# Kernel optimization log

Measured on AMD Instinct MI355X. Metric: run time of the kernel, lower is better.

## Reference

```python
import jax, jax.numpy as jnp
import numpy as np


def setup_inputs() -> dict:
    key = jax.random.key(0)
    k1, k2, k3 = jax.random.split(key, 3)
    dim, heads, dim_head, rows = 512, 8, 64, 64
    b, t = 4, 256
    _dim = heads * dim_head
    x = jax.random.normal(k1, (b * rows, t, dim), dtype=jnp.float32)
    # torch nn.Linear weight layout: [out_features, in_features]
    W_qkv = jax.random.normal(k2, (3 * _dim, dim), dtype=jnp.float32) * (dim ** -0.5)
    W0 = jax.random.normal(k3, (dim, _dim), dtype=jnp.float32) * (_dim ** -0.5)
    return {"x": x, "W_qkv": W_qkv, "W0": W0, "rows": rows, "heads": heads}


def reference(x, W_qkv, W0, rows, heads):
    br, t, dim = x.shape
    b = br // rows
    three_dim = W_qkv.shape[0]
    dim_head = three_dim // (3 * heads)
    scale = (rows * dim_head) ** -0.5

    qkv = x @ W_qkv.T  # [(b*rows), t, 3*heads*dim_head]
    # einops '(b rows) t (d k h) -> k b rows h t d': last dim ordered (d, k, h)
    qkv = qkv.reshape(b, rows, t, dim_head, 3, heads)
    qkv = jnp.transpose(qkv, (4, 0, 1, 5, 2, 3))  # [3, b, rows, h, t, d]
    q, k, v = qkv[0], qkv[1], qkv[2]

    # tied-row attention: sum QK^T over rows before a single shared softmax
    scores = jnp.einsum('brhid,brhjd->bhij', q, k) * scale  # [b, h, t, t]
    attn = jax.nn.softmax(scores, axis=-1)
    # broadcast shared attention map back across rows
    out = jnp.einsum('bhij,brhjd->brhid', attn, v)  # [b, rows, h, t, d]
    # 'b rows h t d -> (b rows) t (h d)'
    out = jnp.transpose(out, (0, 1, 3, 2, 4)).reshape(br, t, heads * dim_head)
    return out @ W0.T
```

## Files before the change

### kernel.cpp

```cpp
#include <hip/hip_runtime.h>


typedef short  bf16x8 __attribute__((ext_vector_type(8)));
typedef float  f32x4  __attribute__((ext_vector_type(4)));

#define MFMA16(a,b,c) __builtin_amdgcn_mfma_f32_16x16x32_bf16((a),(b),(c),0,0,0)

__device__ __forceinline__ ushort f2bf(float f) {
  union { float f; unsigned u; } v; v.f = f;
  unsigned r = v.u + 0x7fffu + ((v.u >> 16) & 1u);
  return (ushort)(r >> 16);
}

__device__ __forceinline__ void gload_lds16(const void* g, void* lds) {
  __builtin_amdgcn_global_load_lds(
      (const __attribute__((address_space(1))) void*)g,
      (__attribute__((address_space(3))) void*)lds, 16, 0, 0);
}


__global__ void cast_f32_to_bf16(const float* __restrict__ in,
                                 ushort* __restrict__ out, int n4) {
  int idx = blockIdx.x * blockDim.x + threadIdx.x;
  int stride = gridDim.x * blockDim.x;
  for (int v = idx; v < n4; v += stride) {
    float4 f = reinterpret_cast<const float4*>(in)[v];
    ushort4 o; o.x = f2bf(f.x); o.y = f2bf(f.y); o.z = f2bf(f.z); o.w = f2bf(f.w);
    reinterpret_cast<ushort4*>(out)[v] = o;
  }
}

__global__ void permute_wqkv_k(const float* __restrict__ W, ushort* __restrict__ Wp) {
  int np = blockIdx.x;
  int k = np >> 9, h = (np >> 6) & 7, d = np & 63;
  const float4* s = reinterpret_cast<const float4*>(W + (size_t)(d * 24 + k * 8 + h) * 512);
  ushort4* o = reinterpret_cast<ushort4*>(Wp + (size_t)np * 512);
  for (int c = threadIdx.x; c < 128; c += blockDim.x) {
    float4 f = s[c];
    ushort4 u; u.x = f2bf(f.x); u.y = f2bf(f.y); u.z = f2bf(f.z); u.w = f2bf(f.w);
    o[c] = u;
  }
}


__device__ __forceinline__ void gemm_nt_256x128(
    const ushort* __restrict__ A, const ushort* __restrict__ B,
    int lda, int ldb, int P, int m0, int n0, char* lds, f32x4 (&acc)[8][4]) {
  const int tid = threadIdx.x;
  const int w = tid >> 6, l = tid & 63;
  const int il = l & 15, kl = l >> 4;
  const int wm = w >> 1, wn = w & 1;

  auto stageA = [&](char* buf, int kt) {
#pragma unroll
    for (int c = 0; c < 4; ++c) {
      int rbase = (w << 6) + (c << 4);
      int row = rbase + (l >> 2);
      int s = ((l & 3) - ((row >> 1) & 3)) & 3;
      gload_lds16(A + (size_t)(m0 + row) * lda + (kt << 5) + (s << 3),
                  buf + rbase * 64);
    }
  };
  auto stageB = [&](char* buf, int kt) {
#pragma unroll
    for (int c = 0; c < 2; ++c) {
      int rbase = (w << 5) + (c << 4);
      int row = rbase + (l >> 2);
      int s = ((l & 3) - ((row >> 1) & 3)) & 3;
      gload_lds16(B + (size_t)(n0 + row) * ldb + (kt << 5) + (s << 3),
                  buf + 16384 + rbase * 64);
    }
  };
  auto loadA8 = [&](const char* buf, bf16x8 (&af)[8]) {
#pragma unroll
    for (int q = 0; q < 8; ++q) {
      int row = (wm << 7) + (q << 4) + il;
      af[q] = *(const bf16x8*)(buf + row * 64 + (((kl + (row >> 1)) & 3) << 4));
    }
  };
  auto loadB4 = [&](const char* buf, bf16x8 (&bfr)[4]) {
#pragma unroll
    for (int q = 0; q < 4; ++q) {
      int row = (wn << 6) + (q << 4) + il;
      bfr[q] = *(const bf16x8*)(buf + 16384 + row * 64 + (((kl + (row >> 1)) & 3) << 4));
    }
  };

#pragma unroll
  for (int i = 0; i < 8; ++i)
#pragma unroll
    for (int j = 0; j < 4; ++j) acc[i][j] = f32x4{0.f, 0.f, 0.f, 0.f};

  stageA(lds, 0);         stageB(lds, 0);
  stageA(lds + 24576, 1); stageB(lds + 24576, 1);
  asm volatile("s_waitcnt vmcnt(6)" ::: "memory");
  __builtin_amdgcn_s_barrier();

  int cur = 0, nx = 2;
  for (int g = 0; g < P; ++g) {
    char* cbuf = lds + cur * 24576;
    char* sbuf = lds + nx * 24576;
    bf16x8 af[8], bfr[4];
    loadA8(cbuf, af);
    loadB4(cbuf, bfr);
    if (g + 2 < P) { stageA(sbuf, g + 2); stageB(sbuf, g + 2); }
    __builtin_amdgcn_s_setprio(1);
#pragma unroll
    for (int fm = 0; fm < 8; ++fm)
#pragma unroll
      for (int fn = 0; fn < 4; ++fn)
        acc[fm][fn] = MFMA16(af[fm], bfr[fn], acc[fm][fn]);
    __builtin_amdgcn_s_setprio(0);
    if (g + 2 < P) asm volatile("s_waitcnt vmcnt(6)" ::: "memory");
    else           asm volatile("s_waitcnt vmcnt(0)" ::: "memory");
    __builtin_amdgcn_s_barrier();
    cur = (cur == 2) ? 0 : cur + 1;
    nx  = (nx  == 2) ? 0 : nx  + 1;
  }
}


__global__ __launch_bounds__(256, 2) void gemm_qkv_k(
    const ushort* __restrict__ xb, const ushort* __restrict__ Wp,
    ushort* __restrict__ Qb, ushort* __restrict__ Kb, ushort* __restrict__ Vt) {
  __shared__ __align__(16) char lds[73728];
  f32x4 acc[8][4];
  const int Bid = blockIdx.x;
  const int xcd = Bid & 7, idx = Bid >> 3;
  const int nt = idx % 12, pl = idx / 12;
  const int m0 = ((pl << 3) + xcd) << 8;
  const int n0 = nt << 7;
  gemm_nt_256x128(xb, Wp, 512, 512, 16, m0, n0, lds, acc);

  const int tid = threadIdx.x, w = tid >> 6, l = tid & 63;
  const int il = l & 15, kl = l >> 4;
  const int wm = w >> 1, wn = w & 1;
  const int kq = n0 >> 9;
  const int br = m0 >> 8, b = br >> 6, r = br & 63;

  if (kq < 2) {
    ushort* dstb = kq ? Kb : Qb;
#pragma unroll
    for (int fm = 0; fm < 8; ++fm)
#pragma unroll
      for (int fn = 0; fn < 4; ++fn) {
        int n = n0 + (wn << 6) + (fn << 4) + il;
        int h = (n >> 6) & 7, d = n & 63;
#pragma unroll
        for (int j = 0; j < 4; ++j) {
          int i = (wm << 7) + (fm << 4) + (kl << 2) + j;
          size_t dst = ((size_t)((((b << 3) + h) << 8) + i) << 12) + (r << 6) + d;
          dstb[dst] = f2bf(acc[fm][fn][j]);
        }
      }
  } else {
#pragma unroll
    for (int fm = 0; fm < 8; ++fm)
#pragma unroll
      for (int fn = 0; fn < 4; ++fn) {
        int n = n0 - 1024 + (wn << 6) + (fn << 4) + il;
        int h = n >> 6, d = n & 63;
        int i0 = (wm << 7) + (fm << 4) + (kl << 2);
        size_t dst = (((size_t)((((b << 3) + h) << 12)) + (r << 6) + d) << 8) + i0;
        ushort4 pk; pk.x = f2bf(acc[fm][fn][0]); pk.y = f2bf(acc[fm][fn][1]);
        pk.z = f2bf(acc[fm][fn][2]); pk.w = f2bf(acc[fm][fn][3]);
        *reinterpret_cast<ushort4*>(&Vt[dst]) = pk;
      }
  }
}


__global__ __launch_bounds__(256, 2) void gemm_out_k(
    const ushort* __restrict__ O2, const ushort* __restrict__ W0b,
    float* __restrict__ out) {
  __shared__ __align__(16) char lds[73728];
  f32x4 acc[8][4];
  const int Bid = blockIdx.x;
  const int xcd = Bid & 7, idx = Bid >> 3;
  const int nt = idx & 3, pl = idx >> 2;
  const int m0 = ((pl << 3) + xcd) << 8;
  const int n0 = nt << 7;
  gemm_nt_256x128(O2, W0b, 512, 512, 16, m0, n0, lds, acc);

  const int tid = threadIdx.x, w = tid >> 6, l = tid & 63;
  const int il = l & 15, kl = l >> 4;
  const int wm = w >> 1, wn = w & 1;
#pragma unroll
  for (int fm = 0; fm < 8; ++fm)
#pragma unroll
    for (int fn = 0; fn < 4; ++fn) {
      int n = n0 + (wn << 6) + (fn << 4) + il;
#pragma unroll
      for (int j = 0; j < 4; ++j) {
        int m = m0 + (wm << 7) + (fm << 4) + (kl << 2) + j;
        out[(size_t)m * 512 + n] = acc[fm][fn][j];
      }
    }
}


__global__ __launch_bounds__(256, 2) void gemm_s_k(
    const ushort* __restrict__ Qb, const ushort* __restrict__ Kb,
    float* __restrict__ Sp) {
  __shared__ __align__(16) char lds[73728];
  f32x4 acc[8][4];
  const int Bid = blockIdx.x;
  const int xcd = Bid & 7, idx = Bid >> 3;
  const int nt = idx & 1, zl = idx >> 1;
  const int z = (zl << 3) + xcd;
  const int bh = z >> 3, ks = z & 7;
  const int n0 = nt << 7;
  const size_t base = ((size_t)bh << 20) + ((size_t)ks << 9);
  gemm_nt_256x128(Qb + base, Kb + base, 4096, 4096, 16, 0, n0, lds, acc);

  const int tid = threadIdx.x, w = tid >> 6, l = tid & 63;
  const int il = l & 15, kl = l >> 4;
  const int wm = w >> 1, wn = w & 1;
  float* o = Sp + ((size_t)z << 16);
#pragma unroll
  for (int fm = 0; fm < 8; ++fm)
#pragma unroll
    for (int fn = 0; fn < 4; ++fn) {
      int n = n0 + (wn << 6) + (fn << 4) + il;
#pragma unroll
      for (int j = 0; j < 4; ++j) {
        int m = (wm << 7) + (fm << 4) + (kl << 2) + j;
        o[(size_t)m * 256 + n] = acc[fm][fn][j];
      }
    }
}


__global__ void softmax_k(const float* __restrict__ Sp, ushort* __restrict__ Pb) {
  const int w = threadIdx.x >> 6, l = threadIdx.x & 63;
  const int row = (blockIdx.x << 2) + w;
  const int bh = row >> 8, i = row & 255;
  const float4* p0 = reinterpret_cast<const float4*>(
      Sp + (((size_t)bh << 3) << 16) + ((size_t)i << 8)) + l;
  float s0 = 0.f, s1 = 0.f, s2 = 0.f, s3 = 0.f;
#pragma unroll
  for (int ks = 0; ks < 8; ++ks) {
    float4 a = p0[(size_t)ks * 16384];
    s0 += a.x; s1 += a.y; s2 += a.z; s3 += a.w;
  }
  const float scale = 0.015625f;
  s0 *= scale; s1 *= scale; s2 *= scale; s3 *= scale;
  float m = fmaxf(fmaxf(s0, s1), fmaxf(s2, s3));
#pragma unroll
  for (int d2 = 1; d2 < 64; d2 <<= 1) m = fmaxf(m, __shfl_xor(m, d2));
  float e0 = __expf(s0 - m), e1 = __expf(s1 - m);
  float e2 = __expf(s2 - m), e3 = __expf(s3 - m);
  float sum = e0 + e1 + e2 + e3;
#pragma unroll
  for (int d2 = 1; d2 < 64; d2 <<= 1) sum += __shfl_xor(sum, d2);
  float r = 1.0f / sum;
  ushort4 p; p.x = f2bf(e0 * r); p.y = f2bf(e1 * r);
  p.z = f2bf(e2 * r); p.w = f2bf(e3 * r);
  reinterpret_cast<ushort4*>(Pb + ((size_t)bh << 16) + ((size_t)i << 8))[l] = p;
}


__global__ __launch_bounds__(256, 2) void gemm_pv_k(
    const ushort* __restrict__ Vt, const ushort* __restrict__ Pb,
    ushort* __restrict__ O2) {
  __shared__ __align__(16) char lds[73728];
  f32x4 acc[8][4];
  const int Bid = blockIdx.x;
  const int xcd = Bid & 7, idx = Bid >> 3;
  const int sub = idx & 31, grp = idx >> 5;
  const int bh = (grp << 3) + xcd, b = bh >> 3, h = bh & 7;
  const int m0 = (sub >> 1) << 8;
  const int n0 = (sub & 1) << 7;
  gemm_nt_256x128(Vt + ((size_t)bh << 20), Pb + ((size_t)bh << 16),
                  256, 256, 8, m0, n0, lds, acc);

  const int tid = threadIdx.x, w = tid >> 6, l = tid & 63;
  const int il = l & 15, kl = l >> 4;
  const int wm = w >> 1, wn = w & 1;
#pragma unroll
  for (int fm = 0; fm < 8; ++fm) {
    int rd0 = m0 + (wm << 7) + (fm << 4) + (kl << 2);
    int r = rd0 >> 6, d0 = rd0 & 63;
#pragma unroll
    for (int fn = 0; fn < 4; ++fn) {
      int i = n0 + (wn << 6) + (fn << 4) + il;
      ushort4 pk; pk.x = f2bf(acc[fm][fn][0]); pk.y = f2bf(acc[fm][fn][1]);
      pk.z = f2bf(acc[fm][fn][2]); pk.w = f2bf(acc[fm][fn][3]);
      *reinterpret_cast<ushort4*>(
          O2 + ((size_t)((((b << 6) + r) << 8) + i) << 9) + (h << 6) + d0) = pk;
    }
  }
}


extern "C" void kernel_launch(void* const* d_in, const int* in_sizes, int n_in,
                              void* d_out, int out_size, void* d_ws, size_t ws_size,
                              hipStream_t stream) {
  const float* x    = (const float*)d_in[0];
  const float* Wqkv = (const float*)d_in[1];
  const float* W0   = (const float*)d_in[2];
  float* out = (float*)d_out;

  char* ws = (char*)d_ws;
  ushort* xb  = (ushort*)(ws);
  ushort* Wp  = (ushort*)(ws + 67108864);
  ushort* W0b = (ushort*)(ws + 68681728);
  ushort* Qb  = (ushort*)(ws + 69206016);
  ushort* Kb  = (ushort*)(ws + 136314880);
  ushort* Vt  = (ushort*)(ws + 203423744);
  if (ws_size < 270532608ull) return;

  cast_f32_to_bf16<<<2048, 256, 0, stream>>>(x, xb, 8388608);
  cast_f32_to_bf16<<<256, 256, 0, stream>>>(W0, W0b, 65536);
  permute_wqkv_k<<<1536, 128, 0, stream>>>(Wqkv, Wp);

  gemm_qkv_k<<<3072, 256, 0, stream>>>(xb, Wp, Qb, Kb, Vt);

  float*  Sp = (float*)xb;
  ushort* Pb = Qb;
  ushort* O2 = xb;

  gemm_s_k<<<512, 256, 0, stream>>>(Qb, Kb, Sp);
  softmax_k<<<2048, 256, 0, stream>>>(Sp, Pb);
  gemm_pv_k<<<1024, 256, 0, stream>>>(Vt, Pb, O2);

  gemm_out_k<<<1024, 256, 0, stream>>>(O2, W0b, out);
}
```

Baseline: 303.5 us.

## Replace GEMM core with 256x256 tile, 8-wave, 8-phase interleaved load/MFMA schedule

Rewrites the shared bf16 NT GEMM routine to use 512-thread blocks computing 256x256 tiles with BK=64. It double-buffers 128KB of LDS and splits each K-step into four sub-phases that interleave partial global-to-LDS staging with MFMA groups, using an 8-way XOR swizzle. All four GEMM kernels change their grids and index mapping to match. The aim is higher arithmetic intensity per tile and better overlap of memory with compute. In exchange, occupancy drops to one block per CU, there are more barriers per K-step, and the per-block register load is heavy.

```diff
diff --git a/kernel.cpp b/kernel.cpp
--- a/kernel.cpp
+++ b/kernel.cpp
@@ -43,47 +43,54 @@
 }
 
 
-__device__ __forceinline__ void gemm_nt_256x128(
+__device__ __forceinline__ void gemm_nt_8phase(
     const ushort* __restrict__ A, const ushort* __restrict__ B,
-    int lda, int ldb, int P, int m0, int n0, char* lds, f32x4 (&acc)[8][4]) {
+    int lda, int ldb, int NT, int m0, int n0, char* lds, f32x4 (&acc)[8][4]) {
   const int tid = threadIdx.x;
   const int w = tid >> 6, l = tid & 63;
   const int il = l & 15, kl = l >> 4;
-  const int wm = w >> 1, wn = w & 1;
-
-  auto stageA = [&](char* buf, int kt) {
-#pragma unroll
-    for (int c = 0; c < 4; ++c) {
-      int rbase = (w << 6) + (c << 4);
-      int row = rbase + (l >> 2);
-      int s = ((l & 3) - ((row >> 1) & 3)) & 3;
-      gload_lds16(A + (size_t)(m0 + row) * lda + (kt << 5) + (s << 3),
-                  buf + rbase * 64);
+  const int wm = w >> 2, wn = w & 3;
+
+  auto stageA = [&](char* buf, int kt, int h) {
+#pragma unroll
+    for (int hh = 0; hh < 2; ++hh) {
+      int rbase = (hh << 7) + (h << 6) + (w << 3);
+      int row = rbase + (l >> 3);
+      int ks = ((l & 7) - row) & 7;
+      gload_lds16(A + (size_t)(m0 + row) * lda + (kt << 6) + (ks << 3),
+                  buf + (size_t)rbase * 128);
     }
   };
-  auto stageB = [&](char* buf, int kt) {
-#pragma unroll
-    for (int c = 0; c < 2; ++c) {
-      int rbase = (w << 5) + (c << 4);
-      int row = rbase + (l >> 2);
-      int s = ((l & 3) - ((row >> 1) & 3)) & 3;
-      gload_lds16(B + (size_t)(n0 + row) * ldb + (kt << 5) + (s << 3),
-                  buf + 16384 + rbase * 64);
+  auto stageB = [&](char* buf, int kt, int c) {
+#pragma unroll
+    for (int c2 = 0; c2 < 2; ++c2) {
+      int rr = (w << 3);
+      int rbase = (c2 << 7) + (((rr >> 5)) << 6) + (c << 5) + (rr & 31);
+      int row = rbase + (l >> 3);
+      int ks = ((l & 7) - row) & 7;
+      gload_lds16(B + (size_t)(n0 + row) * ldb + (kt << 6) + (ks << 3),
+                  buf + 32768 + (size_t)rbase * 128);
     }
   };
-  auto loadA8 = [&](const char* buf, bf16x8 (&af)[8]) {
-#pragma unroll
-    for (int q = 0; q < 8; ++q) {
-      int row = (wm << 7) + (q << 4) + il;
-      af[q] = *(const bf16x8*)(buf + row * 64 + (((kl + (row >> 1)) & 3) << 4));
-    }
+  auto loadA = [&](const char* buf, int h, bf16x8 (&a)[4][2]) {
+#pragma unroll
+    for (int fr4 = 0; fr4 < 4; ++fr4)
+#pragma unroll
+      for (int kk = 0; kk < 2; ++kk) {
+        int row = (wm << 7) + (((h << 2) + fr4) << 4) + il;
+        a[fr4][kk] = *(const bf16x8*)(buf + row * 128 +
+                        ((((kk << 2) + kl + row) & 7) << 4));
+      }
   };
-  auto loadB4 = [&](const char* buf, bf16x8 (&bfr)[4]) {
-#pragma unroll
-    for (int q = 0; q < 4; ++q) {
-      int row = (wn << 6) + (q << 4) + il;
-      bfr[q] = *(const bf16x8*)(buf + 16384 + row * 64 + (((kl + (row >> 1)) & 3) << 4));
-    }
+  auto loadB = [&](const char* buf, int c, bf16x8 (&bb)[2][2]) {
+#pragma unroll
+    for (int fn2 = 0; fn2 < 2; ++fn2)
+#pragma unroll
+      for (int kk = 0; kk < 2; ++kk) {
+        int row = (wn << 6) + (((c << 1) + fn2) << 4) + il;
+        bb[fn2][kk] = *(const bf16x8*)(buf + 32768 + row * 128 +
+                        ((((kk << 2) + kl + row) & 7) << 4));
+      }
   };
 
 #pragma unroll
@@ -91,50 +98,95 @@
 #pragma unroll
     for (int j = 0; j < 4; ++j) acc[i][j] = f32x4{0.f, 0.f, 0.f, 0.f};
 
-  stageA(lds, 0);         stageB(lds, 0);
-  stageA(lds + 24576, 1); stageB(lds + 24576, 1);
+  char* buf0 = lds;
+  char* buf1 = lds + 65536;
+
+  stageA(buf0, 0, 0); stageB(buf0, 0, 0); stageA(buf0, 0, 1); stageB(buf0, 0, 1);
+  stageA(buf1, 1, 0); stageB(buf1, 1, 0); stageA(buf1, 1, 1);
   asm volatile("s_waitcnt vmcnt(6)" ::: "memory");
   __builtin_amdgcn_s_barrier();
 
-  int cur = 0, nx = 2;
-  for (int g = 0; g < P; ++g) {
-    char* cbuf = lds + cur * 24576;
-    char* sbuf = lds + nx * 24576;
-    bf16x8 af[8], bfr[4];
-    loadA8(cbuf, af);
-    loadB4(cbuf, bfr);
-    if (g + 2 < P) { stageA(sbuf, g + 2); stageB(sbuf, g + 2); }
+  for (int g = 0; g < NT; ++g) {
+    char* bc = lds + ((g & 1) << 16);
+    char* bo = lds + (((g & 1) ^ 1) << 16);
+    bf16x8 a[4][2], b0[2][2], b1[2][2];
+
+    loadA(bc, 0, a);
+    loadB(bc, 0, b0);
+    if (g + 1 < NT) stageB(bo, g + 1, 1);
+    __builtin_amdgcn_s_barrier();
     __builtin_amdgcn_s_setprio(1);
 #pragma unroll
-    for (int fm = 0; fm < 8; ++fm)
-#pragma unroll
-      for (int fn = 0; fn < 4; ++fn)
-        acc[fm][fn] = MFMA16(af[fm], bfr[fn], acc[fm][fn]);
+    for (int fr4 = 0; fr4 < 4; ++fr4)
+#pragma unroll
+      for (int fn2 = 0; fn2 < 2; ++fn2)
+#pragma unroll
+        for (int kk = 0; kk < 2; ++kk)
+          acc[fr4][fn2] = MFMA16(a[fr4][kk], b0[fn2][kk], acc[fr4][fn2]);
     __builtin_amdgcn_s_setprio(0);
-    if (g + 2 < P) asm volatile("s_waitcnt vmcnt(6)" ::: "memory");
-    else           asm volatile("s_waitcnt vmcnt(0)" ::: "memory");
-    __builtin_amdgcn_s_barrier();
-    cur = (cur == 2) ? 0 : cur + 1;
-    nx  = (nx  == 2) ? 0 : nx  + 1;
-  }
-}
-
-
-__global__ __launch_bounds__(256, 2) void gemm_qkv_k(
+    __builtin_amdgcn_s_barrier();
+
+    loadB(bc, 1, b1);
+    if (g + 2 < NT) stageA(bc, g + 2, 0);
+    __builtin_amdgcn_s_barrier();
+    __builtin_amdgcn_s_setprio(1);
+#pragma unroll
+    for (int fr4 = 0; fr4 < 4; ++fr4)
+#pragma unroll
+      for (int fn2 = 0; fn2 < 2; ++fn2)
+#pragma unroll
+        for (int kk = 0; kk < 2; ++kk)
+          acc[fr4][2 + fn2] = MFMA16(a[fr4][kk], b1[fn2][kk], acc[fr4][2 + fn2]);
+    __builtin_amdgcn_s_setprio(0);
+    __builtin_amdgcn_s_barrier();
+
+    loadA(bc, 1, a);
+    if (g + 2 < NT) stageB(bc, g + 2, 0);
+    __builtin_amdgcn_s_barrier();
+    __builtin_amdgcn_s_setprio(1);
+#pragma unroll
+    for (int fr4 = 0; fr4 < 4; ++fr4)
+#pragma unroll
+      for (int fn2 = 0; fn2 < 2; ++fn2)
+#pragma unroll
+        for (int kk = 0; kk < 2; ++kk)
+          acc[4 + fr4][fn2] = MFMA16(a[fr4][kk], b0[fn2][kk], acc[4 + fr4][fn2]);
+    __builtin_amdgcn_s_setprio(0);
+    __builtin_amdgcn_s_barrier();
+
+    if (g + 2 < NT) stageA(bc, g + 2, 1);
+    __builtin_amdgcn_s_barrier();
+    __builtin_amdgcn_s_setprio(1);
+#pragma unroll
+    for (int fr4 = 0; fr4 < 4; ++fr4)
+#pragma unroll
+      for (int fn2 = 0; fn2 < 2; ++fn2)
+#pragma unroll
+        for (int kk = 0; kk < 2; ++kk)
+          acc[4 + fr4][2 + fn2] = MFMA16(a[fr4][kk], b1[fn2][kk], acc[4 + fr4][2 + fn2]);
+    __builtin_amdgcn_s_setprio(0);
+    if (g + 2 < NT)      asm volatile("s_waitcnt vmcnt(4)" ::: "memory");
+    else if (g + 1 < NT) asm volatile("s_waitcnt vmcnt(0)" ::: "memory");
+    __builtin_amdgcn_s_barrier();
+  }
+}
+
+
+__global__ __launch_bounds__(512, 1) void gemm_qkv_k(
     const ushort* __restrict__ xb, const ushort* __restrict__ Wp,
     ushort* __restrict__ Qb, ushort* __restrict__ Kb, ushort* __restrict__ Vt) {
-  __shared__ __align__(16) char lds[73728];
+  __shared__ __align__(16) char lds[131072];
   f32x4 acc[8][4];
   const int Bid = blockIdx.x;
   const int xcd = Bid & 7, idx = Bid >> 3;
-  const int nt = idx % 12, pl = idx / 12;
+  const int nt = idx % 6, pl = idx / 6;
   const int m0 = ((pl << 3) + xcd) << 8;
-  const int n0 = nt << 7;
-  gemm_nt_256x128(xb, Wp, 512, 512, 16, m0, n0, lds, acc);
+  const int n0 = nt << 8;
+  gemm_nt_8phase(xb, Wp, 512, 512, 8, m0, n0, lds, acc);
 
   const int tid = threadIdx.x, w = tid >> 6, l = tid & 63;
   const int il = l & 15, kl = l >> 4;
-  const int wm = w >> 1, wn = w & 1;
+  const int wm = w >> 2, wn = w & 3;
   const int kq = n0 >> 9;
   const int br = m0 >> 8, b = br >> 6, r = br & 63;
 
@@ -144,7 +196,7 @@
     for (int fm = 0; fm < 8; ++fm)
 #pragma unroll
       for (int fn = 0; fn < 4; ++fn) {
-        int n = n0 + (wn << 6) + (fn << 4) + il;
+        int n = (n0 & 511) + (wn << 6) + (fn << 4) + il;
         int h = (n >> 6) & 7, d = n & 63;
 #pragma unroll
         for (int j = 0; j < 4; ++j) {
@@ -158,7 +210,7 @@
     for (int fm = 0; fm < 8; ++fm)
 #pragma unroll
       for (int fn = 0; fn < 4; ++fn) {
-        int n = n0 - 1024 + (wn << 6) + (fn << 4) + il;
+        int n = (n0 - 1024) + (wn << 6) + (fn << 4) + il;
         int h = n >> 6, d = n & 63;
         int i0 = (wm << 7) + (fm << 4) + (kl << 2);
         size_t dst = (((size_t)((((b << 3) + h) << 12)) + (r << 6) + d) << 8) + i0;
@@ -170,21 +222,21 @@
 }
 
 
-__global__ __launch_bounds__(256, 2) void gemm_out_k(
+__global__ __launch_bounds__(512, 1) void gemm_out_k(
     const ushort* __restrict__ O2, const ushort* __restrict__ W0b,
     float* __restrict__ out) {
-  __shared__ __align__(16) char lds[73728];
+  __shared__ __align__(16) char lds[131072];
   f32x4 acc[8][4];
   const int Bid = blockIdx.x;
   const int xcd = Bid & 7, idx = Bid >> 3;
-  const int nt = idx & 3, pl = idx >> 2;
+  const int nt = idx & 1, pl = idx >> 1;
   const int m0 = ((pl << 3) + xcd) << 8;
-  const int n0 = nt << 7;
-  gemm_nt_256x128(O2, W0b, 512, 512, 16, m0, n0, lds, acc);
+  const int n0 = nt << 8;
+  gemm_nt_8phase(O2, W0b, 512, 512, 8, m0, n0, lds, acc);
 
   const int tid = threadIdx.x, w = tid >> 6, l = tid & 63;
   const int il = l & 15, kl = l >> 4;
-  const int wm = w >> 1, wn = w & 1;
+  const int wm = w >> 2, wn = w & 3;
 #pragma unroll
   for (int fm = 0; fm < 8; ++fm)
 #pragma unroll
@@ -199,29 +251,25 @@
 }
 
 
-__global__ __launch_bounds__(256, 2) void gemm_s_k(
+__global__ __launch_bounds__(512, 1) void gemm_s_k(
     const ushort* __restrict__ Qb, const ushort* __restrict__ Kb,
     float* __restrict__ Sp) {
-  __shared__ __align__(16) char lds[73728];
+  __shared__ __align__(16) char lds[131072];
   f32x4 acc[8][4];
   const int Bid = blockIdx.x;
-  const int xcd = Bid & 7, idx = Bid >> 3;
-  const int nt = idx & 1, zl = idx >> 1;
-  const int z = (zl << 3) + xcd;
-  const int bh = z >> 3, ks = z & 7;
-  const int n0 = nt << 7;
+  const int bh = Bid & 31, ks = Bid >> 5;
   const size_t base = ((size_t)bh << 20) + ((size_t)ks << 9);
-  gemm_nt_256x128(Qb + base, Kb + base, 4096, 4096, 16, 0, n0, lds, acc);
+  gemm_nt_8phase(Qb + base, Kb + base, 4096, 4096, 8, 0, 0, lds, acc);
 
   const int tid = threadIdx.x, w = tid >> 6, l = tid & 63;
   const int il = l & 15, kl = l >> 4;
-  const int wm = w >> 1, wn = w & 1;
-  float* o = Sp + ((size_t)z << 16);
+  const int wm = w >> 2, wn = w & 3;
+  float* o = Sp + ((size_t)((bh << 3) + ks) << 16);
 #pragma unroll
   for (int fm = 0; fm < 8; ++fm)
 #pragma unroll
     for (int fn = 0; fn < 4; ++fn) {
-      int n = n0 + (wn << 6) + (fn << 4) + il;
+      int n = (wn << 6) + (fn << 4) + il;
 #pragma unroll
       for (int j = 0; j < 4; ++j) {
         int m = (wm << 7) + (fm << 4) + (kl << 2) + j;
@@ -260,30 +308,28 @@
 }
 
 
-__global__ __launch_bounds__(256, 2) void gemm_pv_k(
+__global__ __launch_bounds__(512, 1) void gemm_pv_k(
     const ushort* __restrict__ Vt, const ushort* __restrict__ Pb,
     ushort* __restrict__ O2) {
-  __shared__ __align__(16) char lds[73728];
+  __shared__ __align__(16) char lds[131072];
   f32x4 acc[8][4];
   const int Bid = blockIdx.x;
-  const int xcd = Bid & 7, idx = Bid >> 3;
-  const int sub = idx & 31, grp = idx >> 5;
-  const int bh = (grp << 3) + xcd, b = bh >> 3, h = bh & 7;
-  const int m0 = (sub >> 1) << 8;
-  const int n0 = (sub & 1) << 7;
-  gemm_nt_256x128(Vt + ((size_t)bh << 20), Pb + ((size_t)bh << 16),
-                  256, 256, 8, m0, n0, lds, acc);
+  const int bh = Bid & 31, mt = Bid >> 5;
+  const int b = bh >> 3, h = bh & 7;
+  const int m0 = mt << 8;
+  gemm_nt_8phase(Vt + ((size_t)bh << 20), Pb + ((size_t)bh << 16),
+                 256, 256, 4, m0, 0, lds, acc);
 
   const int tid = threadIdx.x, w = tid >> 6, l = tid & 63;
   const int il = l & 15, kl = l >> 4;
-  const int wm = w >> 1, wn = w & 1;
+  const int wm = w >> 2, wn = w & 3;
 #pragma unroll
   for (int fm = 0; fm < 8; ++fm) {
     int rd0 = m0 + (wm << 7) + (fm << 4) + (kl << 2);
     int r = rd0 >> 6, d0 = rd0 & 63;
 #pragma unroll
     for (int fn = 0; fn < 4; ++fn) {
-      int i = n0 + (wn << 6) + (fn << 4) + il;
+      int i = (wn << 6) + (fn << 4) + il;
       ushort4 pk; pk.x = f2bf(acc[fm][fn][0]); pk.y = f2bf(acc[fm][fn][1]);
       pk.z = f2bf(acc[fm][fn][2]); pk.w = f2bf(acc[fm][fn][3]);
       *reinterpret_cast<ushort4*>(
@@ -314,15 +360,15 @@
   cast_f32_to_bf16<<<256, 256, 0, stream>>>(W0, W0b, 65536);
   permute_wqkv_k<<<1536, 128, 0, stream>>>(Wqkv, Wp);
 
-  gemm_qkv_k<<<3072, 256, 0, stream>>>(xb, Wp, Qb, Kb, Vt);
+  gemm_qkv_k<<<1536, 512, 0, stream>>>(xb, Wp, Qb, Kb, Vt);
 
   float*  Sp = (float*)xb;
   ushort* Pb = Qb;
   ushort* O2 = xb;
 
-  gemm_s_k<<<512, 256, 0, stream>>>(Qb, Kb, Sp);
+  gemm_s_k<<<256, 512, 0, stream>>>(Qb, Kb, Sp);
   softmax_k<<<2048, 256, 0, stream>>>(Sp, Pb);
-  gemm_pv_k<<<1024, 256, 0, stream>>>(Vt, Pb, O2);
-
-  gemm_out_k<<<1024, 256, 0, stream>>>(O2, W0b, out);
-}
+  gemm_pv_k<<<512, 512, 0, stream>>>(Vt, Pb, O2);
+
+  gemm_out_k<<<512, 512, 0, stream>>>(O2, W0b, out);
+}
```

After: 300.9 us. About the same (-0.8%).

## Fuse x bf16 cast into QKV GEMM, merge weight prep, halve S split-K

Applied to the files above, without the earlier changes.

The QKV GEMM now loads fp32 x straight from global memory into registers, converts it to bf16 and writes it into swizzled LDS, replacing the separate cast pass and its 64MB bf16 intermediate. The two weight-prep kernels are merged into one launch. The S GEMM split-K factor drops from 8 to 4, which halves the partial-score traffic the softmax has to read but also halves the S GEMM grid. The A-operand path now goes through registers instead of direct global-to-LDS loads, which raises register pressure and puts more VALU work into the main loop.

```diff
diff --git a/kernel.cpp b/kernel.cpp
--- a/kernel.cpp
+++ b/kernel.cpp
@@ -19,26 +19,26 @@
 }
 
 
-__global__ void cast_f32_to_bf16(const float* __restrict__ in,
-                                 ushort* __restrict__ out, int n4) {
-  int idx = blockIdx.x * blockDim.x + threadIdx.x;
-  int stride = gridDim.x * blockDim.x;
-  for (int v = idx; v < n4; v += stride) {
-    float4 f = reinterpret_cast<const float4*>(in)[v];
-    ushort4 o; o.x = f2bf(f.x); o.y = f2bf(f.y); o.z = f2bf(f.z); o.w = f2bf(f.w);
-    reinterpret_cast<ushort4*>(out)[v] = o;
-  }
-}
-
-__global__ void permute_wqkv_k(const float* __restrict__ W, ushort* __restrict__ Wp) {
-  int np = blockIdx.x;
-  int k = np >> 9, h = (np >> 6) & 7, d = np & 63;
-  const float4* s = reinterpret_cast<const float4*>(W + (size_t)(d * 24 + k * 8 + h) * 512);
-  ushort4* o = reinterpret_cast<ushort4*>(Wp + (size_t)np * 512);
-  for (int c = threadIdx.x; c < 128; c += blockDim.x) {
-    float4 f = s[c];
+__global__ void prep_k(const float* __restrict__ W, ushort* __restrict__ Wp,
+                       const float* __restrict__ W0, ushort* __restrict__ W0b) {
+  const int bid = blockIdx.x, tid = threadIdx.x;
+  if (bid < 768) {
+    int np = (bid << 1) + (tid >> 7);
+    int c  = tid & 127;
+    int k = np >> 9, h = (np >> 6) & 7, d = np & 63;
+    float4 f = reinterpret_cast<const float4*>(
+        W + (size_t)(d * 24 + k * 8 + h) * 512)[c];
     ushort4 u; u.x = f2bf(f.x); u.y = f2bf(f.y); u.z = f2bf(f.z); u.w = f2bf(f.w);
-    o[c] = u;
+    reinterpret_cast<ushort4*>(Wp + (size_t)np * 512)[c] = u;
+  } else {
+    int v0 = ((bid - 768) << 10) + (tid << 2);
+#pragma unroll
+    for (int q = 0; q < 4; ++q) {
+      int v = v0 + q;
+      float4 f = reinterpret_cast<const float4*>(W0)[v];
+      ushort4 u; u.x = f2bf(f.x); u.y = f2bf(f.y); u.z = f2bf(f.z); u.w = f2bf(f.w);
+      reinterpret_cast<ushort4*>(W0b)[v] = u;
+    }
   }
 }
 
@@ -121,23 +121,106 @@
 
 
 __global__ __launch_bounds__(256, 2) void gemm_qkv_k(
-    const ushort* __restrict__ xb, const ushort* __restrict__ Wp,
+    const float* __restrict__ x, const ushort* __restrict__ Wp,
     ushort* __restrict__ Qb, ushort* __restrict__ Kb, ushort* __restrict__ Vt) {
-  __shared__ __align__(16) char lds[73728];
+  __shared__ __align__(16) char lds_s[73728];
+  char* lds = lds_s;
   f32x4 acc[8][4];
   const int Bid = blockIdx.x;
   const int xcd = Bid & 7, idx = Bid >> 3;
   const int nt = idx % 12, pl = idx / 12;
   const int m0 = ((pl << 3) + xcd) << 8;
   const int n0 = nt << 7;
-  gemm_nt_256x128(xb, Wp, 512, 512, 16, m0, n0, lds, acc);
 
   const int tid = threadIdx.x, w = tid >> 6, l = tid & 63;
   const int il = l & 15, kl = l >> 4;
   const int wm = w >> 1, wn = w & 1;
+
+  float4 ar[8];
+  auto loadAx = [&](int kt) {
+#pragma unroll
+    for (int rd = 0; rd < 8; ++rd) {
+      int row = (rd << 5) + (w << 3) + (l >> 3);
+      ar[rd] = *reinterpret_cast<const float4*>(
+          x + (size_t)(m0 + row) * 512 + (kt << 5) + ((l & 7) << 2));
+    }
+  };
+  auto writeA = [&](char* buf) {
+#pragma unroll
+    for (int rd = 0; rd < 8; ++rd) {
+      int row = (rd << 5) + (w << 3) + (l >> 3);
+      int c = l & 7;
+      int slot = (((c >> 1) + (row >> 1)) & 3);
+      ushort4 h;
+      h.x = f2bf(ar[rd].x); h.y = f2bf(ar[rd].y);
+      h.z = f2bf(ar[rd].z); h.w = f2bf(ar[rd].w);
+      *reinterpret_cast<ushort4*>(buf + row * 64 + (slot << 4) + ((c & 1) << 3)) = h;
+    }
+  };
+  auto stageB = [&](char* buf, int kt) {
+#pragma unroll
+    for (int c = 0; c < 2; ++c) {
+      int rbase = (w << 5) + (c << 4);
+      int row = rbase + (l >> 2);
+      int s = ((l & 3) - ((row >> 1) & 3)) & 3;
+      gload_lds16(Wp + (size_t)(n0 + row) * 512 + (kt << 5) + (s << 3),
+                  buf + 16384 + rbase * 64);
+    }
+  };
+  auto loadA8 = [&](const char* buf, bf16x8 (&af)[8]) {
+#pragma unroll
+    for (int q = 0; q < 8; ++q) {
+      int row = (wm << 7) + (q << 4) + il;
+      af[q] = *(const bf16x8*)(buf + row * 64 + (((kl + (row >> 1)) & 3) << 4));
+    }
+  };
+  auto loadB4 = [&](const char* buf, bf16x8 (&bfr)[4]) {
+#pragma unroll
+    for (int q = 0; q < 4; ++q) {
+      int row = (wn << 6) + (q << 4) + il;
+      bfr[q] = *(const bf16x8*)(buf + 16384 + row * 64 + (((kl + (row >> 1)) & 3) << 4));
+    }
+  };
+
+#pragma unroll
+  for (int i = 0; i < 8; ++i)
+#pragma unroll
+    for (int j = 0; j < 4; ++j) acc[i][j] = f32x4{0.f, 0.f, 0.f, 0.f};
+
+  loadAx(0);
+  asm volatile("s_waitcnt vmcnt(0)" ::: "memory");
+  writeA(lds);
+  loadAx(1);
+  stageB(lds, 0); stageB(lds + 24576, 1);
+  asm volatile("s_waitcnt vmcnt(2)" ::: "memory");
+  asm volatile("s_waitcnt lgkmcnt(0)" ::: "memory");
+  __builtin_amdgcn_s_barrier();
+
+  int cur = 0;
+  for (int g = 0; g < 16; ++g) {
+    int wn1 = (cur == 2) ? 0 : cur + 1;
+    int nx2 = (wn1 == 2) ? 0 : wn1 + 1;
+    if (g + 1 < 16) writeA(lds + wn1 * 24576);
+    bf16x8 af[8], bfr[4];
+    loadA8(lds + cur * 24576, af);
+    loadB4(lds + cur * 24576, bfr);
+    if (g + 2 < 16) { loadAx(g + 2); stageB(lds + nx2 * 24576, g + 2); }
+    __builtin_amdgcn_s_setprio(1);
+#pragma unroll
+    for (int fm = 0; fm < 8; ++fm)
+#pragma unroll
+      for (int fn = 0; fn < 4; ++fn)
+        acc[fm][fn] = MFMA16(af[fm], bfr[fn], acc[fm][fn]);
+    __builtin_amdgcn_s_setprio(0);
+    if (g + 2 < 16) asm volatile("s_waitcnt vmcnt(2)" ::: "memory");
+    else            asm volatile("s_waitcnt vmcnt(0)" ::: "memory");
+    asm volatile("s_waitcnt lgkmcnt(0)" ::: "memory");
+    __builtin_amdgcn_s_barrier();
+    cur = wn1;
+  }
+
   const int kq = n0 >> 9;
   const int br = m0 >> 8, b = br >> 6, r = br & 63;
-
   if (kq < 2) {
     ushort* dstb = kq ? Kb : Qb;
 #pragma unroll
@@ -205,13 +288,11 @@
   __shared__ __align__(16) char lds[73728];
   f32x4 acc[8][4];
   const int Bid = blockIdx.x;
-  const int xcd = Bid & 7, idx = Bid >> 3;
-  const int nt = idx & 1, zl = idx >> 1;
-  const int z = (zl << 3) + xcd;
-  const int bh = z >> 3, ks = z & 7;
+  const int nt = Bid & 1, z = Bid >> 1;
+  const int bh = z >> 2, ks = z & 3;
   const int n0 = nt << 7;
-  const size_t base = ((size_t)bh << 20) + ((size_t)ks << 9);
-  gemm_nt_256x128(Qb + base, Kb + base, 4096, 4096, 16, 0, n0, lds, acc);
+  const size_t base = ((size_t)bh << 20) + ((size_t)ks << 10);
+  gemm_nt_256x128(Qb + base, Kb + base, 4096, 4096, 32, 0, n0, lds, acc);
 
   const int tid = threadIdx.x, w = tid >> 6, l = tid & 63;
   const int il = l & 15, kl = l >> 4;
@@ -236,15 +317,13 @@
   const int row = (blockIdx.x << 2) + w;
   const int bh = row >> 8, i = row & 255;
   const float4* p0 = reinterpret_cast<const float4*>(
-      Sp + (((size_t)bh << 3) << 16) + ((size_t)i << 8)) + l;
-  float s0 = 0.f, s1 = 0.f, s2 = 0.f, s3 = 0.f;
-#pragma unroll
-  for (int ks = 0; ks < 8; ++ks) {
-    float4 a = p0[(size_t)ks * 16384];
-    s0 += a.x; s1 += a.y; s2 += a.z; s3 += a.w;
-  }
+      Sp + (((size_t)bh << 2) << 16) + ((size_t)i << 8)) + l;
+  float4 a = p0[0], b2 = p0[16384], c = p0[32768], d = p0[49152];
   const float scale = 0.015625f;
-  s0 *= scale; s1 *= scale; s2 *= scale; s3 *= scale;
+  float s0 = (a.x + b2.x + c.x + d.x) * scale;
+  float s1 = (a.y + b2.y + c.y + d.y) * scale;
+  float s2 = (a.z + b2.z + c.z + d.z) * scale;
+  float s3 = (a.w + b2.w + c.w + d.w) * scale;
   float m = fmaxf(fmaxf(s0, s1), fmaxf(s2, s3));
 #pragma unroll
   for (int d2 = 1; d2 < 64; d2 <<= 1) m = fmaxf(m, __shfl_xor(m, d2));
@@ -302,7 +381,6 @@
   float* out = (float*)d_out;
 
   char* ws = (char*)d_ws;
-  ushort* xb  = (ushort*)(ws);
   ushort* Wp  = (ushort*)(ws + 67108864);
   ushort* W0b = (ushort*)(ws + 68681728);
   ushort* Qb  = (ushort*)(ws + 69206016);
@@ -310,17 +388,15 @@
   ushort* Vt  = (ushort*)(ws + 203423744);
   if (ws_size < 270532608ull) return;
 
-  cast_f32_to_bf16<<<2048, 256, 0, stream>>>(x, xb, 8388608);
-  cast_f32_to_bf16<<<256, 256, 0, stream>>>(W0, W0b, 65536);
-  permute_wqkv_k<<<1536, 128, 0, stream>>>(Wqkv, Wp);
-
-  gemm_qkv_k<<<3072, 256, 0, stream>>>(xb, Wp, Qb, Kb, Vt);
-
-  float*  Sp = (float*)xb;
+  prep_k<<<832, 256, 0, stream>>>(Wqkv, Wp, W0, W0b);
+
+  gemm_qkv_k<<<3072, 256, 0, stream>>>(x, Wp, Qb, Kb, Vt);
+
+  float*  Sp = (float*)ws;
   ushort* Pb = Qb;
-  ushort* O2 = xb;
-
-  gemm_s_k<<<512, 256, 0, stream>>>(Qb, Kb, Sp);
+  ushort* O2 = (ushort*)ws;
+
+  gemm_s_k<<<256, 256, 0, stream>>>(Qb, Kb, Sp);
   softmax_k<<<2048, 256, 0, stream>>>(Sp, Pb);
   gemm_pv_k<<<1024, 256, 0, stream>>>(Vt, Pb, O2);
 
```

Measured after the change: 334.7 us. 10.3% more time.
